# Kernel tuning notes

Measured on AMD Instinct MI355X. Metric: run time of the kernel, lower is better.

## Reference

```python
import jax, jax.numpy as jnp
import numpy as np

B, L_Q, L_K, H, D = 8, 2048, 2048, 8, 64
FACTOR = 5
U_PART = max(1, min(FACTOR * int(np.ceil(np.log(L_K + 1))), L_K))  # sample_k = 40
U_TOP = max(1, min(FACTOR * int(np.ceil(np.log(L_Q + 1))), L_Q))   # n_top = 40


def setup_inputs() -> dict:
    key = jax.random.key(0)
    kq, kk, kv, ki = jax.random.split(key, 4)
    queries = jax.random.normal(kq, (B, L_Q, H, D), dtype=jnp.float32)
    keys = jax.random.normal(kk, (B, L_K, H, D), dtype=jnp.float32)
    values = jax.random.normal(kv, (B, L_K, H, D), dtype=jnp.float32)
    # random key-sampling indices (GPU randint in the torch module), shared across B,H
    index_sample = jax.random.randint(ki, (L_Q, U_PART), 0, L_K)
    return {"queries": queries, "keys": keys, "values": values,
            "index_sample": index_sample}


def reference(queries, keys, values, index_sample):
    b, l_q, h, d = queries.shape
    l_k = keys.shape[1]
    # [B, L, H, D] -> [B, H, L, D]
    Q = jnp.transpose(queries, (0, 2, 1, 3))
    K = jnp.transpose(keys, (0, 2, 1, 3))
    V = jnp.transpose(values, (0, 2, 1, 3))

    # --- _prob_QK: sparse sampling + sparsity-measure topk query selection ---
    K_sample = K[:, :, index_sample, :]                     # [B,H,L_Q,S,D]
    Q_K_sample = jnp.einsum('bhqe,bhqse->bhqs', Q, K_sample)
    M = Q_K_sample.max(axis=-1) - Q_K_sample.mean(axis=-1)  # [B,H,L_Q]
    _, M_top = jax.lax.top_k(M, U_TOP)                      # [B,H,u] query indices
    Q_reduce = jnp.take_along_axis(Q, M_top[..., None], axis=2)  # [B,H,u,D]
    scores = jnp.einsum('bhue,bhke->bhuk', Q_reduce, K)     # [B,H,u,L_K]
    scores = scores * (1.0 / np.sqrt(d))

    # --- causal mask for selected queries (mask_flag=True) ---
    key_pos = jnp.arange(l_k)
    causal = key_pos[None, None, None, :] > M_top[..., None]  # key > query pos
    scores = jnp.where(causal, -jnp.inf, scores)

    attn = jax.nn.softmax(scores, axis=-1)                  # dropout in eval mode
    attn_out = jnp.einsum('bhuk,bhkd->bhud', attn, V)       # [B,H,u,D]

    # --- initial context (causal => cumulative sum of V) + scatter update ---
    context = jnp.cumsum(V, axis=2)                         # [B,H,L_Q,D]
    b_idx = jnp.arange(b)[:, None, None]
    h_idx = jnp.arange(h)[None, :, None]
    context = context.at[b_idx, h_idx, M_top].set(attn_out)

    return jnp.transpose(context, (0, 2, 1, 3))             # [B,L_Q,H,D]
```

## Files before the change

### kernel.cpp

```cpp
#include <hip/hip_runtime.h>
#include <math.h>

#define Bb 8
#define Hh 8
#define LQ 2048
#define LK 2048
#define Dd 64
#define Uu 40
#define NCH 64
#define CHUNK (LK / NCH)
#define NSPL 8
#define CK (LK / NSPL)
#define SM_BLOCKS (Bb * (LQ / 8))
#define PART_BLOCKS (Bb * NCH / 2)

typedef float f32x4 __attribute__((ext_vector_type(4)));
typedef short bf16x8 __attribute__((ext_vector_type(8)));

__device__ __forceinline__ float dot4(float4 a, float4 b) {
    return a.x * b.x + a.y * b.y + a.z * b.z + a.w * b.w;
}

__device__ __forceinline__ short f2bf(float x) {
    unsigned u = __float_as_uint(x);
    unsigned r = u + 0x7fffu + ((u >> 16) & 1u);
    return (short)(r >> 16);
}

__device__ __forceinline__ bf16x8 pack8(float4 a, float4 b) {
    bf16x8 r;
    r[0] = f2bf(a.x); r[1] = f2bf(a.y); r[2] = f2bf(a.z); r[3] = f2bf(a.w);
    r[4] = f2bf(b.x); r[5] = f2bf(b.y); r[6] = f2bf(b.z); r[7] = f2bf(b.w);
    return r;
}

__global__ __launch_bounds__(256) void k_sampleM(
    const float* __restrict__ Qp, const float* __restrict__ Kp,
    const int* __restrict__ idxs, const float* __restrict__ Vp,
    float* __restrict__ M, float* __restrict__ part)
{
    int t = threadIdx.x;

    if (blockIdx.x >= SM_BLOCKS) {
        int bid2 = blockIdx.x - SM_BLOCKS;
        int b = bid2 >> 5;
        int c = (bid2 & 31) * 2 + (t >> 7);
        int h = (t >> 4) & 7, d4 = (t & 15) * 4;

        const float* vb = Vp + ((size_t)(b * LK + c * CHUNK)) * 512 + h * 64 + d4;
        float4 s = make_float4(0.f, 0.f, 0.f, 0.f);
#pragma unroll 4
        for (int l = 0; l < CHUNK; ++l) {
            float4 v = *reinterpret_cast<const float4*>(vb + (size_t)l * 512);
            s.x += v.x; s.y += v.y; s.z += v.z; s.w += v.w;
        }
        int bh = b * 8 + h;
        *reinterpret_cast<float4*>(&part[(size_t)(bh * NCH + c) * Dd + d4]) = s;
        return;
    }

    int b  = blockIdx.x & 7;
    int qt = blockIdx.x >> 3;
    int lane = t & 63, wave = t >> 6;

    __shared__ int sIdx[8 * Uu];
    for (int i = t; i < 8 * Uu; i += 256)
        sIdx[i] = idxs[(qt * 8) * Uu + i];
    __syncthreads();

    const size_t HD = 512;
    const float* Kb = Kp + (size_t)b * LK * HD + lane * 4;

#pragma unroll
    for (int i = 0; i < 2; ++i) {
        int lq = wave * 2 + i;
        int q  = qt * 8 + lq;
        const int* sI = &sIdx[lq * Uu];
#pragma unroll
        for (int ph = 0; ph < 2; ++ph) {
            f32x4 qa = __builtin_nontemporal_load(
                reinterpret_cast<const f32x4*>(
                    Qp + ((size_t)b * LQ + q) * HD + ph * 256) + lane);

            float mx = -INFINITY, sm = 0.f;
#pragma unroll 8
            for (int s = 0; s < Uu; ++s) {
                int kidx = sI[s];
                f32x4 kv = *reinterpret_cast<const f32x4*>(
                    Kb + (size_t)kidx * HD + ph * 256);
                float p = qa[0] * kv[0] + qa[1] * kv[1]
                        + qa[2] * kv[2] + qa[3] * kv[3];
                p += __shfl_xor(p, 1, 64);
                p += __shfl_xor(p, 2, 64);
                p += __shfl_xor(p, 4, 64);
                p += __shfl_xor(p, 8, 64);
                mx = fmaxf(mx, p); sm += p;
            }
            if ((lane & 15) == 0) {
                int h = ph * 4 + (lane >> 4);
                __builtin_nontemporal_store(
                    mx - sm * (1.0f / Uu), &M[((b * 8 + h) << 11) + q]);
            }
        }
    }
}

__global__ __launch_bounds__(64) void k_topk_prefix(
    const float* __restrict__ M, int* __restrict__ Mtop, int* __restrict__ sel,
    float* __restrict__ part)
{
    if (blockIdx.x >= Bb * Hh) {
        int bh = blockIdx.x - Bb * Hh;
        int d = threadIdx.x;
        float run = 0.f;
        for (int c = 0; c < NCH; ++c) {
            size_t i = (size_t)(bh * NCH + c) * Dd + d;
            float tmp = part[i];
            part[i] = run;
            run += tmp;
        }
        return;
    }

    int bh = blockIdx.x;
    int lane = threadIdx.x;
    __shared__ float Ml[LQ];

    for (int j = lane; j < LQ; j += 64) {
        Ml[j] = M[bh * LQ + j];
        sel[bh * LQ + j] = -1;
    }
    __syncthreads();

    float lv = -INFINITY; int li = LQ;
    for (int j = 0; j < 32; ++j) {
        int idx = lane + 64 * j;
        float x = Ml[idx];
        if (x > lv) { lv = x; li = idx; }
    }

    for (int u = 0; u < Uu; ++u) {
        float v = lv; int id = li;
#pragma unroll
        for (int off = 32; off > 0; off >>= 1) {
            float ov = __shfl_xor(v, off, 64);
            int   oi = __shfl_xor(id, off, 64);
            if (ov > v || (ov == v && oi < id)) { v = ov; id = oi; }
        }
        if (lane == 0) {
            Mtop[bh * Uu + u] = id;
            sel[bh * LQ + id] = u;
        }
        if ((id & 63) == lane) {
            Ml[id] = -INFINITY;
            lv = -INFINITY; li = LQ;
            for (int j = 0; j < 32; ++j) {
                int idx = lane + 64 * j;
                float x = Ml[idx];
                if (x > lv) { lv = x; li = idx; }
            }
        }
    }
}

__global__ __launch_bounds__(256) void k_attn_part(
    const float* __restrict__ Qp, const float* __restrict__ Kp,
    const float* __restrict__ Vp, const int* __restrict__ Mtop,
    float* __restrict__ pacc, float* __restrict__ pl)
{
    int bh = blockIdx.x >> 3;
    int c  = blockIdx.x & (NSPL - 1);
    int b = bh >> 3, h = bh & 7;
    int t = threadIdx.x;
    int lane = t & 63, w = t >> 6;
    int col = lane & 15, hi = lane >> 4;

    __shared__ int sP[48];
    __shared__ __align__(16) short sPl[2][48][80];
    __shared__ float sL[4][48];

    if (t < 48) sP[t] = (t < Uu) ? Mtop[bh * Uu + t] : -1;
    __syncthreads();

    int pmax = 0;
#pragma unroll 8
    for (int u = 0; u < Uu; ++u) pmax = max(pmax, sP[u]);

    bf16x8 qf[3][2];
#pragma unroll
    for (int qb = 0; qb < 3; ++qb) {
        int q = qb * 16 + col;
        int row = sP[q];
#pragma unroll
        for (int ks = 0; ks < 2; ++ks) {
            const float* qp = Qp + (((size_t)b * LQ + max(row, 0)) * Hh + h) * Dd
                              + ks * 32 + hi * 8;
            float4 x = *reinterpret_cast<const float4*>(qp);
            float4 y = *reinterpret_cast<const float4*>(qp + 4);
            bf16x8 f = pack8(x, y);
            if (row < 0) f = (bf16x8)(short)0;
            qf[qb][ks] = f;
        }
    }

    f32x4 oacc[3];
    float lsum[3];
#pragma unroll
    for (int qb = 0; qb < 3; ++qb) { oacc[qb] = (f32x4)0.f; lsum[qb] = 0.f; }

    for (int tt = 0; tt < CK / 64; ++tt) {
        int k0 = c * CK + tt * 64;
        if (pmax < k0) break;
        int pb = tt & 1;

        bf16x8 af[2];
#pragma unroll
        for (int ks = 0; ks < 2; ++ks) {
            const float* kp = Kp + (((size_t)b * LK + k0 + 16 * w + col) * Hh + h) * Dd
                              + ks * 32 + hi * 8;
            float4 x = *reinterpret_cast<const float4*>(kp);
            float4 y = *reinterpret_cast<const float4*>(kp + 4);
            af[ks] = pack8(x, y);
        }

#pragma unroll
        for (int qb = 0; qb < 3; ++qb) {
            f32x4 s = (f32x4)0.f;
            s = __builtin_amdgcn_mfma_f32_16x16x32_bf16(af[0], qf[qb][0], s, 0, 0, 0);
            s = __builtin_amdgcn_mfma_f32_16x16x32_bf16(af[1], qf[qb][1], s, 0, 0, 0);

            int p = sP[qb * 16 + col];
            int kbase = k0 + 16 * w + hi * 4;
            float e0 = (kbase + 0 <= p) ? __expf(s[0] * 0.125f) : 0.f;
            float e1 = (kbase + 1 <= p) ? __expf(s[1] * 0.125f) : 0.f;
            float e2 = (kbase + 2 <= p) ? __expf(s[2] * 0.125f) : 0.f;
            float e3 = (kbase + 3 <= p) ? __expf(s[3] * 0.125f) : 0.f;
            lsum[qb] += (e0 + e1) + (e2 + e3);

            int q = qb * 16 + col;
            int kl = 16 * w + hi * 4;
            unsigned p01 = (unsigned)(unsigned short)f2bf(e0)
                         | ((unsigned)(unsigned short)f2bf(e1) << 16);
            unsigned p23 = (unsigned)(unsigned short)f2bf(e2)
                         | ((unsigned)(unsigned short)f2bf(e3) << 16);
            *reinterpret_cast<unsigned*>(&sPl[pb][q][kl])     = p01;
            *reinterpret_cast<unsigned*>(&sPl[pb][q][kl + 2]) = p23;
        }
        __syncthreads();

#pragma unroll
        for (int ks = 0; ks < 2; ++ks) {
            const float* vb = Vp + (((size_t)b * LK + k0 + ks * 32 + hi * 8) * Hh + h) * Dd
                              + 16 * w + col;
            float4 x, y;
            x.x = vb[0];       x.y = vb[512];      x.z = vb[1024];     x.w = vb[1536];
            y.x = vb[2048];    y.y = vb[2560];     y.z = vb[3072];     y.w = vb[3584];
            bf16x8 vf = pack8(x, y);
#pragma unroll
            for (int qb = 0; qb < 3; ++qb) {
                bf16x8 pf = *reinterpret_cast<const bf16x8*>(
                    &sPl[pb][qb * 16 + col][ks * 32 + hi * 8]);
                oacc[qb] = __builtin_amdgcn_mfma_f32_16x16x32_bf16(pf, vf, oacc[qb], 0, 0, 0);
            }
        }
    }

#pragma unroll
    for (int qb = 0; qb < 3; ++qb) {
#pragma unroll
        for (int r = 0; r < 4; ++r) {
            int q = qb * 16 + hi * 4 + r;
            if (q < Uu)
                pacc[(((size_t)bh * NSPL + c) * Uu + q) * Dd + 16 * w + col] = oacc[qb][r];
        }
        lsum[qb] += __shfl_xor(lsum[qb], 16, 64);
        lsum[qb] += __shfl_xor(lsum[qb], 32, 64);
        if (lane < 16) sL[w][qb * 16 + lane] = lsum[qb];
    }
    __syncthreads();
    if (t < Uu)
        pl[((size_t)bh * NSPL + c) * Uu + t] =
            sL[0][t] + sL[1][t] + sL[2][t] + sL[3][t];
}

__global__ __launch_bounds__(128) void k_scan(
    const float* __restrict__ Vp, const float* __restrict__ part,
    const int* __restrict__ sel, const float* __restrict__ pacc,
    const float* __restrict__ pl, float* __restrict__ out)
{
    int c = blockIdx.x & (NCH - 1);
    int b = blockIdx.x >> 6;
    int g = threadIdx.x;
    int h = g >> 4, d4 = (g & 15) * 4;
    int bh = b * 8 + h;

    float4 run = *reinterpret_cast<const float4*>(
        &part[(size_t)(bh * NCH + c) * Dd + d4]);

    int l0 = c * CHUNK;
    const float* vb = Vp + ((size_t)(b * LK + l0)) * 512 + h * 64 + d4;
    float* ob = out + ((size_t)(b * LQ + l0)) * 512 + h * 64 + d4;
    const int* sb = sel + bh * LQ + l0;

#pragma unroll 4
    for (int l = 0; l < CHUNK; ++l) {
        float4 v = *reinterpret_cast<const float4*>(vb + (size_t)l * 512);
        run.x += v.x; run.y += v.y; run.z += v.z; run.w += v.w;
        int s = sb[l];
        float4 o = run;
        if (s >= 0) {
            float4 A = make_float4(0.f, 0.f, 0.f, 0.f);
            float L = 0.f;
#pragma unroll
            for (int cc = 0; cc < NSPL; ++cc) {
                float4 pa = *reinterpret_cast<const float4*>(
                    &pacc[(((size_t)bh * NSPL + cc) * Uu + s) * Dd + d4]);
                A.x += pa.x; A.y += pa.y; A.z += pa.z; A.w += pa.w;
                L += pl[((size_t)bh * NSPL + cc) * Uu + s];
            }
            float inv = 1.0f / L;
            o = make_float4(A.x * inv, A.y * inv, A.z * inv, A.w * inv);
        }
        *reinterpret_cast<float4*>(ob + (size_t)l * 512) = o;
    }
}

extern "C" void kernel_launch(void* const* d_in, const int* in_sizes, int n_in,
                              void* d_out, int out_size, void* d_ws, size_t ws_size,
                              hipStream_t stream) {
    const float* Qp   = (const float*)d_in[0];
    const float* Kp   = (const float*)d_in[1];
    const float* Vp   = (const float*)d_in[2];
    const int*   idxs = (const int*)d_in[3];
    float* out = (float*)d_out;

    char* w = (char*)d_ws;
    float* M    = (float*)(w);
    int*   sel  = (int*)  (w + 512 * 1024);
    int*   Mtop = (int*)  (w + 1024 * 1024);
    float* part = (float*)(w + 1040 * 1024);
    float* pacc = (float*)(w + 2064 * 1024);
    float* pl   = (float*)(w + 7184 * 1024);

    k_sampleM<<<SM_BLOCKS + PART_BLOCKS, 256, 0, stream>>>(Qp, Kp, idxs, Vp, M, part);
    k_topk_prefix<<<2 * Bb * Hh, 64, 0, stream>>>(M, Mtop, sel, part);
    k_attn_part<<<Bb * Hh * NSPL, 256, 0, stream>>>(Qp, Kp, Vp, Mtop, pacc, pl);
    k_scan<<<Bb * NCH, 128, 0, stream>>>(Vp, part, sel, pacc, pl, out);
}
```

Before: 151.4 us.

## Overlap cumsum scan with attention and scatter selected rows in fixup kernel

```diff
diff --git a/kernel.cpp b/kernel.cpp
--- a/kernel.cpp
+++ b/kernel.cpp
@@ -13,13 +13,11 @@
 #define CK (LK / NSPL)
 #define SM_BLOCKS (Bb * (LQ / 8))
 #define PART_BLOCKS (Bb * NCH / 2)
+#define ATTN_BLOCKS (Bb * Hh * NSPL)
+#define SCAN_BLOCKS (Bb * NCH / 2)
 
 typedef float f32x4 __attribute__((ext_vector_type(4)));
 typedef short bf16x8 __attribute__((ext_vector_type(8)));
-
-__device__ __forceinline__ float dot4(float4 a, float4 b) {
-    return a.x * b.x + a.y * b.y + a.z * b.z + a.w * b.w;
-}
 
 __device__ __forceinline__ short f2bf(float x) {
     unsigned u = __float_as_uint(x);
@@ -34,15 +32,15 @@
     return r;
 }
 
-__global__ __launch_bounds__(256) void k_sampleM(
+__global__ __launch_bounds__(256) void k_main(
     const float* __restrict__ Qp, const float* __restrict__ Kp,
     const int* __restrict__ idxs, const float* __restrict__ Vp,
     float* __restrict__ M, float* __restrict__ part)
 {
     int t = threadIdx.x;
 
-    if (blockIdx.x >= SM_BLOCKS) {
-        int bid2 = blockIdx.x - SM_BLOCKS;
+    if (blockIdx.x < PART_BLOCKS) {
+        int bid2 = blockIdx.x;
         int b = bid2 >> 5;
         int c = (bid2 & 31) * 2 + (t >> 7);
         int h = (t >> 4) & 7, d4 = (t & 15) * 4;
@@ -59,8 +57,9 @@
         return;
     }
 
-    int b  = blockIdx.x & 7;
-    int qt = blockIdx.x >> 3;
+    int bid = blockIdx.x - PART_BLOCKS;
+    int b  = bid & 7;
+    int qt = bid >> 3;
     int lane = t & 63, wave = t >> 6;
 
     __shared__ int sIdx[8 * Uu];
@@ -105,31 +104,15 @@
     }
 }
 
-__global__ __launch_bounds__(64) void k_topk_prefix(
-    const float* __restrict__ M, int* __restrict__ Mtop, int* __restrict__ sel,
-    float* __restrict__ part)
+__global__ __launch_bounds__(64) void k_topk(
+    const float* __restrict__ M, int* __restrict__ Mtop)
 {
-    if (blockIdx.x >= Bb * Hh) {
-        int bh = blockIdx.x - Bb * Hh;
-        int d = threadIdx.x;
-        float run = 0.f;
-        for (int c = 0; c < NCH; ++c) {
-            size_t i = (size_t)(bh * NCH + c) * Dd + d;
-            float tmp = part[i];
-            part[i] = run;
-            run += tmp;
-        }
-        return;
-    }
-
     int bh = blockIdx.x;
     int lane = threadIdx.x;
     __shared__ float Ml[LQ];
 
-    for (int j = lane; j < LQ; j += 64) {
+    for (int j = lane; j < LQ; j += 64)
         Ml[j] = M[bh * LQ + j];
-        sel[bh * LQ + j] = -1;
-    }
     __syncthreads();
 
     float lv = -INFINITY; int li = LQ;
@@ -147,10 +130,8 @@
             int   oi = __shfl_xor(id, off, 64);
             if (ov > v || (ov == v && oi < id)) { v = ov; id = oi; }
         }
-        if (lane == 0) {
+        if (lane == 0)
             Mtop[bh * Uu + u] = id;
-            sel[bh * LQ + id] = u;
-        }
         if ((id & 63) == lane) {
             Ml[id] = -INFINITY;
             lv = -INFINITY; li = LQ;
@@ -163,15 +144,44 @@
     }
 }
 
-__global__ __launch_bounds__(256) void k_attn_part(
+__global__ __launch_bounds__(256) void k_attn_scan(
     const float* __restrict__ Qp, const float* __restrict__ Kp,
     const float* __restrict__ Vp, const int* __restrict__ Mtop,
-    float* __restrict__ pacc, float* __restrict__ pl)
+    const float* __restrict__ part, float* __restrict__ pacc,
+    float* __restrict__ pl, float* __restrict__ out)
 {
+    int t = threadIdx.x;
+
+    if (blockIdx.x >= ATTN_BLOCKS) {
+        int bid2 = blockIdx.x - ATTN_BLOCKS;
+        int b = bid2 >> 5;
+        int ch = (bid2 & 31) * 2 + (t >> 7);
+        int t2 = t & 127;
+        int h = t2 >> 4, d4 = (t2 & 15) * 4;
+        int bh = b * 8 + h;
+
+        float4 run = make_float4(0.f, 0.f, 0.f, 0.f);
+        for (int cc = 0; cc < ch; ++cc) {
+            float4 p4 = *reinterpret_cast<const float4*>(
+                &part[(size_t)(bh * NCH + cc) * Dd + d4]);
+            run.x += p4.x; run.y += p4.y; run.z += p4.z; run.w += p4.w;
+        }
+
+        int l0 = ch * CHUNK;
+        const float* vb = Vp + ((size_t)(b * LK + l0)) * 512 + h * 64 + d4;
+        float* ob = out + ((size_t)(b * LQ + l0)) * 512 + h * 64 + d4;
+#pragma unroll 4
+        for (int l = 0; l < CHUNK; ++l) {
+            float4 v = *reinterpret_cast<const float4*>(vb + (size_t)l * 512);
+            run.x += v.x; run.y += v.y; run.z += v.z; run.w += v.w;
+            *reinterpret_cast<float4*>(ob + (size_t)l * 512) = run;
+        }
+        return;
+    }
+
     int bh = blockIdx.x >> 3;
     int c  = blockIdx.x & (NSPL - 1);
     int b = bh >> 3, h = bh & 7;
-    int t = threadIdx.x;
     int lane = t & 63, w = t >> 6;
     int col = lane & 15, hi = lane >> 4;
 
@@ -283,46 +293,23 @@
             sL[0][t] + sL[1][t] + sL[2][t] + sL[3][t];
 }
 
-__global__ __launch_bounds__(128) void k_scan(
-    const float* __restrict__ Vp, const float* __restrict__ part,
-    const int* __restrict__ sel, const float* __restrict__ pacc,
+__global__ __launch_bounds__(256) void k_fixup(
+    const int* __restrict__ Mtop, const float* __restrict__ pacc,
     const float* __restrict__ pl, float* __restrict__ out)
 {
-    int c = blockIdx.x & (NCH - 1);
-    int b = blockIdx.x >> 6;
-    int g = threadIdx.x;
-    int h = g >> 4, d4 = (g & 15) * 4;
-    int bh = b * 8 + h;
-
-    float4 run = *reinterpret_cast<const float4*>(
-        &part[(size_t)(bh * NCH + c) * Dd + d4]);
-
-    int l0 = c * CHUNK;
-    const float* vb = Vp + ((size_t)(b * LK + l0)) * 512 + h * 64 + d4;
-    float* ob = out + ((size_t)(b * LQ + l0)) * 512 + h * 64 + d4;
-    const int* sb = sel + bh * LQ + l0;
-
-#pragma unroll 4
-    for (int l = 0; l < CHUNK; ++l) {
-        float4 v = *reinterpret_cast<const float4*>(vb + (size_t)l * 512);
-        run.x += v.x; run.y += v.y; run.z += v.z; run.w += v.w;
-        int s = sb[l];
-        float4 o = run;
-        if (s >= 0) {
-            float4 A = make_float4(0.f, 0.f, 0.f, 0.f);
-            float L = 0.f;
-#pragma unroll
-            for (int cc = 0; cc < NSPL; ++cc) {
-                float4 pa = *reinterpret_cast<const float4*>(
-                    &pacc[(((size_t)bh * NSPL + cc) * Uu + s) * Dd + d4]);
-                A.x += pa.x; A.y += pa.y; A.z += pa.z; A.w += pa.w;
-                L += pl[((size_t)bh * NSPL + cc) * Uu + s];
-            }
-            float inv = 1.0f / L;
-            o = make_float4(A.x * inv, A.y * inv, A.z * inv, A.w * inv);
-        }
-        *reinterpret_cast<float4*>(ob + (size_t)l * 512) = o;
-    }
+    int gid = blockIdx.x * 4 + (threadIdx.x >> 6);
+    int lane = threadIdx.x & 63;
+    int bh = gid / Uu, u = gid % Uu;
+    int b = bh >> 3, h = bh & 7;
+    int p = Mtop[bh * Uu + u];
+
+    float A = 0.f, L = 0.f;
+#pragma unroll
+    for (int cc = 0; cc < NSPL; ++cc) {
+        A += pacc[(((size_t)bh * NSPL + cc) * Uu + u) * Dd + lane];
+        L += pl[((size_t)bh * NSPL + cc) * Uu + u];
+    }
+    out[(((size_t)b * LQ + p) * Hh + h) * Dd + lane] = A / L;
 }
 
 extern "C" void kernel_launch(void* const* d_in, const int* in_sizes, int n_in,
@@ -336,14 +323,14 @@
 
     char* w = (char*)d_ws;
     float* M    = (float*)(w);
-    int*   sel  = (int*)  (w + 512 * 1024);
-    int*   Mtop = (int*)  (w + 1024 * 1024);
-    float* part = (float*)(w + 1040 * 1024);
-    float* pacc = (float*)(w + 2064 * 1024);
-    float* pl   = (float*)(w + 7184 * 1024);
-
-    k_sampleM<<<SM_BLOCKS + PART_BLOCKS, 256, 0, stream>>>(Qp, Kp, idxs, Vp, M, part);
-    k_topk_prefix<<<2 * Bb * Hh, 64, 0, stream>>>(M, Mtop, sel, part);
-    k_attn_part<<<Bb * Hh * NSPL, 256, 0, stream>>>(Qp, Kp, Vp, Mtop, pacc, pl);
-    k_scan<<<Bb * NCH, 128, 0, stream>>>(Vp, part, sel, pacc, pl, out);
-}
+    int*   Mtop = (int*)  (w + 512 * 1024);
+    float* part = (float*)(w + 528 * 1024);
+    float* pacc = (float*)(w + 1552 * 1024);
+    float* pl   = (float*)(w + 6672 * 1024);
+
+    k_main<<<PART_BLOCKS + SM_BLOCKS, 256, 0, stream>>>(Qp, Kp, idxs, Vp, M, part);
+    k_topk<<<Bb * Hh, 64, 0, stream>>>(M, Mtop);
+    k_attn_scan<<<ATTN_BLOCKS + SCAN_BLOCKS, 256, 0, stream>>>(
+        Qp, Kp, Vp, Mtop, part, pacc, pl, out);
+    k_fixup<<<Bb * Hh * Uu / 4, 256, 0, stream>>>(Mtop, pacc, pl, out);
+}
```

Measured after the change: 154.1 us. About the same (+1.8%).
